# Kernel optimization log

Measured on AMD Instinct MI355X. Metric: run time of the kernel, lower is better.

The kernel has to match this reference:

```python
import jax, jax.numpy as jnp
import numpy as np

NEG_SLOPE = 0.2  # PyG GATConv default leaky_relu slope
EPS = 1e-16


def layer_norm(x, g, b):
    mu = x.mean(-1, keepdims=True)
    var = ((x - mu) ** 2).mean(-1, keepdims=True)
    return (x - mu) * jax.lax.rsqrt(var + 1e-5) * g + b


def gat_conv(x, src, dst, n, W, a_src, a_dst, bias):
    # x: [N, C_in]; W: [C_in, H*C]; a_src/a_dst: [H, C]; concat=False -> mean over heads
    H, C = a_src.shape
    xh = (x @ W).reshape(n, H, C)                      # [N, H, C]
    s_src = jnp.einsum('nhc,hc->nh', xh, a_src)         # [N, H]
    s_dst = jnp.einsum('nhc,hc->nh', xh, a_dst)         # [N, H]
    e = jax.nn.leaky_relu(s_src[src] + s_dst[dst], NEG_SLOPE)  # [E, H]
    # segment softmax over incoming edges of each destination node
    m = jax.ops.segment_max(e, dst, num_segments=n)     # [N, H]
    ee = jnp.exp(e - m[dst])
    z = jax.ops.segment_sum(ee, dst, num_segments=n)    # [N, H]
    alpha = ee / (z[dst] + EPS)                         # [E, H]
    msg = xh[src] * alpha[:, :, None]                   # [E, H, C]
    out = jax.ops.segment_sum(msg, dst, num_segments=n) # [N, H, C]
    return out.mean(axis=1) + bias                      # [N, C]


def setup_inputs() -> dict:
    key = jax.random.key(0)
    N, E, C, H, L = 50000, 400000, 64, 4, 2
    ks = jax.random.split(key, 16)
    x = jax.random.normal(ks[0], (N, C), dtype=jnp.float32)
    edge_index = jax.random.randint(ks[1], (2, E), 0, N, dtype=jnp.int64)
    sc = 1.0 / np.sqrt(C)
    return {
        'x': x,
        'edge_index': edge_index,
        'Wg': jax.random.normal(ks[2], (L, C, H * C), dtype=jnp.float32) * sc,
        'att_src': jax.random.normal(ks[3], (L, H, C), dtype=jnp.float32) * sc,
        'att_dst': jax.random.normal(ks[4], (L, H, C), dtype=jnp.float32) * sc,
        'att_bias': jnp.zeros((L, C), dtype=jnp.float32),
        'ln1_g': jnp.ones((L, C), dtype=jnp.float32),
        'ln1_b': jnp.zeros((L, C), dtype=jnp.float32),
        'W1': jax.random.normal(ks[5], (L, C, C), dtype=jnp.float32) * sc,
        'b1': jnp.zeros((L, C), dtype=jnp.float32),
        'W2': jax.random.normal(ks[6], (L, C, C), dtype=jnp.float32) * sc,
        'b2': jnp.zeros((L, C), dtype=jnp.float32),
        'ln2_g': jnp.ones((L, C), dtype=jnp.float32),
        'ln2_b': jnp.zeros((L, C), dtype=jnp.float32),
    }


def reference(x, edge_index, Wg, att_src, att_dst, att_bias,
              ln1_g, ln1_b, W1, b1, W2, b2, ln2_g, ln2_b):
    n = x.shape[0]
    L = Wg.shape[0]
    # PyG GATConv adds self loops by default
    loops = jnp.arange(n, dtype=edge_index.dtype)
    src = jnp.concatenate([edge_index[0], loops])
    dst = jnp.concatenate([edge_index[1], loops])
    for i in range(L):
        x_att = gat_conv(x, src, dst, n, Wg[i], att_src[i], att_dst[i], att_bias[i])
        x = layer_norm(x + x_att, ln1_g[i], ln1_b[i])
        h = jax.nn.relu(x @ W1[i] + b1[i])
        h = h @ W2[i] + b2[i]
        x = layer_norm(x + h, ln2_g[i], ln2_b[i])
    return x
```

## Files before the change

### kernel.cpp

```cpp
#include <hip/hip_runtime.h>
#include <hip/hip_bf16.h>
#include <float.h>

#define C 64
#define H 4
#define HC 256
#define NEG_SLOPE 0.2f
#define EPS_SEG 1e-16f
#define LN_EPS 1e-5f
#define LDSP 528

typedef __attribute__((ext_vector_type(8))) short bf16x8;
typedef __attribute__((ext_vector_type(4))) float f32x4;

__device__ __forceinline__ float warp_sum(float v) {
#pragma unroll
    for (int m = 32; m >= 1; m >>= 1) v += __shfl_xor(v, m, 64);
    return v;
}

__device__ __forceinline__ unsigned short f2bf(float f) {
    unsigned int u = __float_as_uint(f);
    return (unsigned short)((u + 0x7FFF + ((u >> 16) & 1)) >> 16);
}


__global__ void k_zero(int* __restrict__ a, int n) {
    int i = blockIdx.x * blockDim.x + threadIdx.x;
    int stride = gridDim.x * blockDim.x;
    for (int j = i; j < n; j += stride) a[j] = 0;
}

__global__ void k_count(const int* __restrict__ ei, int* __restrict__ counts,
                        int E, int Etot) {
    int eid = blockIdx.x * blockDim.x + threadIdx.x;
    if (eid >= Etot) return;
    int d = (eid < E) ? ei[E + eid] : eid - E;
    atomicAdd(&counts[d], 1);
}

__global__ __launch_bounds__(256) void k_scan1(const int* __restrict__ counts,
                                               int* __restrict__ tmp,
                                               int* __restrict__ bsum, int N) {
    __shared__ int sm[256];
    int t = threadIdx.x;
    int i = blockIdx.x * 256 + t;
    sm[t] = (i < N) ? counts[i] : 0;
    __syncthreads();
    for (int off = 1; off < 256; off <<= 1) {
        int add = (t >= off) ? sm[t - off] : 0;
        __syncthreads();
        sm[t] += add;
        __syncthreads();
    }
    if (i < N) tmp[i] = sm[t];
    if (t == 255) bsum[blockIdx.x] = sm[255];
}

__global__ __launch_bounds__(256) void k_scan2(int* __restrict__ bsum, int nb) {
    __shared__ int sm[256];
    int t = threadIdx.x;
    sm[t] = (t < nb) ? bsum[t] : 0;
    __syncthreads();
    for (int off = 1; off < 256; off <<= 1) {
        int add = (t >= off) ? sm[t - off] : 0;
        __syncthreads();
        sm[t] += add;
        __syncthreads();
    }
    if (t < nb) bsum[t] = (t > 0) ? sm[t - 1] : 0;
}

__global__ __launch_bounds__(256) void k_scan3(const int* __restrict__ tmp,
                                               const int* __restrict__ boff,
                                               int* __restrict__ rowptr,
                                               int* __restrict__ cursor, int N) {
    int i = blockIdx.x * 256 + threadIdx.x;
    if (i < N) {
        rowptr[i + 1] = tmp[i] + boff[blockIdx.x];
        cursor[i] = 0;
    }
    if (i == 0) rowptr[0] = 0;
}

__global__ void k_fill(const int* __restrict__ ei, const int* __restrict__ rowptr,
                       int* __restrict__ cursor, int* __restrict__ col,
                       int E, int Etot) {
    int eid = blockIdx.x * blockDim.x + threadIdx.x;
    if (eid >= Etot) return;
    int s, d;
    if (eid < E) { s = ei[eid]; d = ei[E + eid]; } else { s = d = eid - E; }
    int pos = rowptr[d] + atomicAdd(&cursor[d], 1);
    col[pos] = s;
}


__global__ void k_prep_x(const float4* __restrict__ xin, ushort4* __restrict__ xb,
                         int n4, int npad4) {
    int i = blockIdx.x * blockDim.x + threadIdx.x;
    int st = gridDim.x * blockDim.x;
    for (int j = i; j < npad4; j += st) {
        ushort4 o;
        if (j < n4) {
            float4 v = xin[j];
            o.x = f2bf(v.x); o.y = f2bf(v.y); o.z = f2bf(v.z); o.w = f2bf(v.w);
        } else {
            o.x = o.y = o.z = o.w = 0;
        }
        xb[j] = o;
    }
}

__global__ void k_prep_weights(const float* __restrict__ Wg,
                               const float* __restrict__ W1, const float* __restrict__ W2,
                               unsigned short* __restrict__ Wgt,
                               unsigned short* __restrict__ W1t,
                               unsigned short* __restrict__ W2t, int L) {
    int i = blockIdx.x * 256 + threadIdx.x;
    int nWg = L * C * HC;
    int nW = L * C * C;
    if (i < nWg) {
        int l = i / (C * HC);
        int r = i - l * C * HC;
        int n = r >> 6, k = r & 63;
        Wgt[(size_t)l * HC * C + n * C + k] = f2bf(Wg[(size_t)l * C * HC + k * HC + n]);
    } else if (i < nWg + nW) {
        int j = i - nWg;
        int l = j / (C * C);
        int r = j - l * C * C;
        int n = r >> 6, k = r & 63;
        W1t[(size_t)l * C * C + n * C + k] = f2bf(W1[(size_t)l * C * C + k * C + n]);
        W2t[(size_t)l * C * C + n * C + k] = f2bf(W2[(size_t)l * C * C + k * C + n]);
    }
}

__global__ __launch_bounds__(256) void k_gemm_mfma(
    const unsigned short* __restrict__ xb, const unsigned short* __restrict__ Wgt,
    const float* __restrict__ a_src, const float* __restrict__ a_dst,
    unsigned short* __restrict__ xh, float* __restrict__ s_src,
    float* __restrict__ s_dst, int N)
{
    __shared__ char tile[64 * LDSP];
    int w = threadIdx.x >> 6, l = threadIdx.x & 63;
    int n0 = blockIdx.x * 64;
    int lr = l & 15, q = l >> 4, lk = q * 8;
    bf16x8 bfr[4][2];
    float as[4], ad[4];
#pragma unroll
    for (int ct = 0; ct < 4; ct++) {
        int colg = w * 64 + ct * 16 + lr;
#pragma unroll
        for (int ks = 0; ks < 2; ks++)
            bfr[ct][ks] = *reinterpret_cast<const bf16x8*>(Wgt + colg * C + ks * 32 + lk);
        as[ct] = a_src[w * C + ct * 16 + lr];
        ad[ct] = a_dst[w * C + ct * 16 + lr];
    }
#pragma unroll
    for (int rt = 0; rt < 4; rt++) {
        const unsigned short* arow = xb + (size_t)(n0 + rt * 16 + lr) * C + lk;
        bf16x8 a0 = *reinterpret_cast<const bf16x8*>(arow);
        bf16x8 a1 = *reinterpret_cast<const bf16x8*>(arow + 32);
        f32x4 acc[4];
#pragma unroll
        for (int ct = 0; ct < 4; ct++) {
            acc[ct] = (f32x4){0.f, 0.f, 0.f, 0.f};
            acc[ct] = __builtin_amdgcn_mfma_f32_16x16x32_bf16(a0, bfr[ct][0], acc[ct], 0, 0, 0);
            acc[ct] = __builtin_amdgcn_mfma_f32_16x16x32_bf16(a1, bfr[ct][1], acc[ct], 0, 0, 0);
        }
        int rowl = rt * 16 + q * 4;
#pragma unroll
        for (int ct = 0; ct < 4; ct++) {
            int cb = (w * 64 + ct * 16 + lr) * 2;
#pragma unroll
            for (int r = 0; r < 4; r++)
                *(unsigned short*)(tile + (rowl + r) * LDSP + cb) = f2bf(acc[ct][r]);
        }
#pragma unroll
        for (int r = 0; r < 4; r++) {
            float ps = acc[0][r] * as[0] + acc[1][r] * as[1]
                     + acc[2][r] * as[2] + acc[3][r] * as[3];
            float pd = acc[0][r] * ad[0] + acc[1][r] * ad[1]
                     + acc[2][r] * ad[2] + acc[3][r] * ad[3];
#pragma unroll
            for (int off = 1; off < 16; off <<= 1) {
                ps += __shfl_xor(ps, off, 64);
                pd += __shfl_xor(pd, off, 64);
            }
            if (lr == 0) {
                int n = n0 + rowl + r;
                s_src[(size_t)n * H + w] = ps;
                s_dst[(size_t)n * H + w] = pd;
            }
        }
    }
    __syncthreads();
#pragma unroll
    for (int it = 0; it < 8; it++) {
        int off = threadIdx.x * 16 + it * 4096;
        int row = off >> 9;
        int cin = off & 511;
        uint4 v = *(const uint4*)(tile + row * LDSP + cin);
        *(uint4*)((char*)xh + (size_t)(n0 + row) * 512 + cin) = v;
    }
}

__global__ __launch_bounds__(256) void k_gat_node(
    const int* __restrict__ rowptr, const int* __restrict__ col,
    const float* __restrict__ s_src, const float* __restrict__ s_dst,
    const unsigned short* __restrict__ xh,
    const float* __restrict__ x_in, const float* __restrict__ bias,
    const float* __restrict__ g, const float* __restrict__ b,
    float* __restrict__ x1, unsigned short* __restrict__ x1b, int N)
{
    int n = (blockIdx.x * blockDim.x + threadIdx.x) >> 6;
    int l = threadIdx.x & 63;
    int h = l >> 4, gq = l & 15;
    if (n >= N) return;
    int r0 = rowptr[n], r1 = rowptr[n + 1];

    float4 xi = *(const float4*)(x_in + (size_t)n * C + gq * 4);
    float4 bia = *(const float4*)(bias + gq * 4);
    float sdh = s_dst[n * H + h];

    const char* xbase = (const char*)xh;
    int laneoff = h * 128 + gq * 8;

    float a0 = 0.f, a1 = 0.f, a2 = 0.f, a3 = 0.f, z = 0.f;

    int j = r0;
    for (; j + 4 <= r1; j += 4) {
        int s0 = col[j], s1 = col[j + 1], s2 = col[j + 2], s3 = col[j + 3];
        uint2 v0 = *(const uint2*)(xbase + (size_t)s0 * 512 + laneoff);
        uint2 v1 = *(const uint2*)(xbase + (size_t)s1 * 512 + laneoff);
        uint2 v2 = *(const uint2*)(xbase + (size_t)s2 * 512 + laneoff);
        uint2 v3 = *(const uint2*)(xbase + (size_t)s3 * 512 + laneoff);
        float e0 = s_src[s0 * H + h] + sdh;
        float e1 = s_src[s1 * H + h] + sdh;
        float e2 = s_src[s2 * H + h] + sdh;
        float e3 = s_src[s3 * H + h] + sdh;
        float w0 = __expf(fmaxf(e0, NEG_SLOPE * e0));
        float w1 = __expf(fmaxf(e1, NEG_SLOPE * e1));
        float w2 = __expf(fmaxf(e2, NEG_SLOPE * e2));
        float w3 = __expf(fmaxf(e3, NEG_SLOPE * e3));
        a0 += w0 * __uint_as_float(v0.x << 16);
        a1 += w0 * __uint_as_float(v0.x & 0xFFFF0000u);
        a2 += w0 * __uint_as_float(v0.y << 16);
        a3 += w0 * __uint_as_float(v0.y & 0xFFFF0000u);
        a0 += w1 * __uint_as_float(v1.x << 16);
        a1 += w1 * __uint_as_float(v1.x & 0xFFFF0000u);
        a2 += w1 * __uint_as_float(v1.y << 16);
        a3 += w1 * __uint_as_float(v1.y & 0xFFFF0000u);
        a0 += w2 * __uint_as_float(v2.x << 16);
        a1 += w2 * __uint_as_float(v2.x & 0xFFFF0000u);
        a2 += w2 * __uint_as_float(v2.y << 16);
        a3 += w2 * __uint_as_float(v2.y & 0xFFFF0000u);
        a0 += w3 * __uint_as_float(v3.x << 16);
        a1 += w3 * __uint_as_float(v3.x & 0xFFFF0000u);
        a2 += w3 * __uint_as_float(v3.y << 16);
        a3 += w3 * __uint_as_float(v3.y & 0xFFFF0000u);
        z += w0 + w1 + w2 + w3;
    }
    {
        int t = r1 - j;
        int s0 = 0, s1 = 0, s2 = 0;
        if (t > 0) s0 = col[j];
        if (t > 1) s1 = col[j + 1];
        if (t > 2) s2 = col[j + 2];
        uint2 v0 = {0, 0}, v1 = {0, 0}, v2 = {0, 0};
        float e0 = 0.f, e1 = 0.f, e2 = 0.f;
        if (t > 0) { v0 = *(const uint2*)(xbase + (size_t)s0 * 512 + laneoff); e0 = s_src[s0 * H + h] + sdh; }
        if (t > 1) { v1 = *(const uint2*)(xbase + (size_t)s1 * 512 + laneoff); e1 = s_src[s1 * H + h] + sdh; }
        if (t > 2) { v2 = *(const uint2*)(xbase + (size_t)s2 * 512 + laneoff); e2 = s_src[s2 * H + h] + sdh; }
        float w0 = (t > 0) ? __expf(fmaxf(e0, NEG_SLOPE * e0)) : 0.f;
        float w1 = (t > 1) ? __expf(fmaxf(e1, NEG_SLOPE * e1)) : 0.f;
        float w2 = (t > 2) ? __expf(fmaxf(e2, NEG_SLOPE * e2)) : 0.f;
        a0 += w0 * __uint_as_float(v0.x << 16);
        a1 += w0 * __uint_as_float(v0.x & 0xFFFF0000u);
        a2 += w0 * __uint_as_float(v0.y << 16);
        a3 += w0 * __uint_as_float(v0.y & 0xFFFF0000u);
        a0 += w1 * __uint_as_float(v1.x << 16);
        a1 += w1 * __uint_as_float(v1.x & 0xFFFF0000u);
        a2 += w1 * __uint_as_float(v1.y << 16);
        a3 += w1 * __uint_as_float(v1.y & 0xFFFF0000u);
        a0 += w2 * __uint_as_float(v2.x << 16);
        a1 += w2 * __uint_as_float(v2.x & 0xFFFF0000u);
        a2 += w2 * __uint_as_float(v2.y << 16);
        a3 += w2 * __uint_as_float(v2.y & 0xFFFF0000u);
        z += w0 + w1 + w2;
    }

    float inv = 0.25f / (z + EPS_SEG);
    a0 *= inv; a1 *= inv; a2 *= inv; a3 *= inv;
#pragma unroll
    for (int off = 16; off <= 32; off <<= 1) {
        a0 += __shfl_xor(a0, off, 64);
        a1 += __shfl_xor(a1, off, 64);
        a2 += __shfl_xor(a2, off, 64);
        a3 += __shfl_xor(a3, off, 64);
    }
    float y0 = xi.x + a0 + bia.x;
    float y1 = xi.y + a1 + bia.y;
    float y2 = xi.z + a2 + bia.z;
    float y3 = xi.w + a3 + bia.w;
    float mu = warp_sum(y0 + y1 + y2 + y3) * (1.f / (C * 4));
    float d0 = y0 - mu, d1 = y1 - mu, d2 = y2 - mu, d3 = y3 - mu;
    float var = warp_sum(d0 * d0 + d1 * d1 + d2 * d2 + d3 * d3) * (1.f / (C * 4));
    float rs = rsqrtf(var + LN_EPS);
    if (h == 0) {
        float4 gg = *(const float4*)(g + gq * 4);
        float4 bb = *(const float4*)(b + gq * 4);
        float4 o;
        o.x = d0 * rs * gg.x + bb.x;
        o.y = d1 * rs * gg.y + bb.y;
        o.z = d2 * rs * gg.z + bb.z;
        o.w = d3 * rs * gg.w + bb.w;
        *(float4*)(x1 + (size_t)n * C + gq * 4) = o;
        ushort4 ob;
        ob.x = f2bf(o.x); ob.y = f2bf(o.y); ob.z = f2bf(o.z); ob.w = f2bf(o.w);
        *(ushort4*)(x1b + (size_t)n * C + gq * 4) = ob;
    }
}

__global__ __launch_bounds__(256) void k_ffn_mfma(
    const float* __restrict__ x1f, const unsigned short* __restrict__ x1b,
    const unsigned short* __restrict__ W1t, const unsigned short* __restrict__ W2t,
    const float* __restrict__ b1, const float* __restrict__ b2,
    const float* __restrict__ g, const float* __restrict__ b,
    float* __restrict__ xout, unsigned short* __restrict__ xb, int N)
{
    __shared__ unsigned short hls[64 * 64];
    int w = threadIdx.x >> 6, l = threadIdx.x & 63;
    int lr = l & 15, q = l >> 4, lk = q * 8;
    int n0 = blockIdx.x * 64;

    {
        bf16x8 bf[4][2];
#pragma unroll
        for (int ct = 0; ct < 4; ct++)
#pragma unroll
            for (int ks = 0; ks < 2; ks++)
                bf[ct][ks] = *reinterpret_cast<const bf16x8*>(
                    W1t + (ct * 16 + lr) * C + ks * 32 + lk);
        const unsigned short* arow = x1b + (size_t)(n0 + w * 16 + lr) * C + lk;
        bf16x8 a0 = *reinterpret_cast<const bf16x8*>(arow);
        bf16x8 a1 = *reinterpret_cast<const bf16x8*>(arow + 32);
        f32x4 acc[4];
#pragma unroll
        for (int ct = 0; ct < 4; ct++) {
            acc[ct] = (f32x4){0.f, 0.f, 0.f, 0.f};
            acc[ct] = __builtin_amdgcn_mfma_f32_16x16x32_bf16(a0, bf[ct][0], acc[ct], 0, 0, 0);
            acc[ct] = __builtin_amdgcn_mfma_f32_16x16x32_bf16(a1, bf[ct][1], acc[ct], 0, 0, 0);
        }
#pragma unroll
        for (int ct = 0; ct < 4; ct++) {
            float bc = b1[ct * 16 + lr];
#pragma unroll
            for (int r = 0; r < 4; r++) {
                float v = fmaxf(acc[ct][r] + bc, 0.f);
                int rowb = w * 16 + q * 4 + r;
                int byte = rowb * 128 + (ct * 16 + lr) * 2;
                byte ^= (rowb & 7) << 4;
                *(unsigned short*)((char*)hls + byte) = f2bf(v);
            }
        }
    }
    __syncthreads();

    bf16x8 bf[4][2];
#pragma unroll
    for (int ct = 0; ct < 4; ct++)
#pragma unroll
        for (int ks = 0; ks < 2; ks++)
            bf[ct][ks] = *reinterpret_cast<const bf16x8*>(
                W2t + (ct * 16 + lr) * C + ks * 32 + lk);
    bf16x8 h0, h1;
    {
        int rowb = w * 16 + lr;
        int swz = (rowb & 7) << 4;
        int byte0 = (rowb * 128 + q * 16) ^ swz;
        int byte1 = (rowb * 128 + 64 + q * 16) ^ swz;
        h0 = *(bf16x8*)((char*)hls + byte0);
        h1 = *(bf16x8*)((char*)hls + byte1);
    }
    f32x4 acc[4];
#pragma unroll
    for (int ct = 0; ct < 4; ct++) {
        acc[ct] = (f32x4){0.f, 0.f, 0.f, 0.f};
        acc[ct] = __builtin_amdgcn_mfma_f32_16x16x32_bf16(h0, bf[ct][0], acc[ct], 0, 0, 0);
        acc[ct] = __builtin_amdgcn_mfma_f32_16x16x32_bf16(h1, bf[ct][1], acc[ct], 0, 0, 0);
    }

    float b2c[4], gc[4], bc[4];
#pragma unroll
    for (int ct = 0; ct < 4; ct++) {
        int cg = ct * 16 + lr;
        b2c[ct] = b2[cg]; gc[ct] = g[cg]; bc[ct] = b[cg];
    }
    float yv[4][4];
#pragma unroll
    for (int r = 0; r < 4; r++) {
        int n = n0 + w * 16 + q * 4 + r;
        bool ok = n < N;
#pragma unroll
        for (int ct = 0; ct < 4; ct++) {
            float xr = ok ? x1f[(size_t)n * C + ct * 16 + lr] : 0.f;
            yv[ct][r] = acc[ct][r] + b2c[ct] + xr;
        }
    }
#pragma unroll
    for (int r = 0; r < 4; r++) {
        int n = n0 + w * 16 + q * 4 + r;
        float s = yv[0][r] + yv[1][r] + yv[2][r] + yv[3][r];
#pragma unroll
        for (int off = 1; off < 16; off <<= 1) s += __shfl_xor(s, off, 64);
        float mu = s * (1.f / C);
        float d0 = yv[0][r] - mu, d1 = yv[1][r] - mu;
        float d2 = yv[2][r] - mu, d3 = yv[3][r] - mu;
        float vs = d0 * d0 + d1 * d1 + d2 * d2 + d3 * d3;
#pragma unroll
        for (int off = 1; off < 16; off <<= 1) vs += __shfl_xor(vs, off, 64);
        float rs = rsqrtf(vs * (1.f / C) + LN_EPS);
        if (n < N) {
            float dd[4] = {d0, d1, d2, d3};
#pragma unroll
            for (int ct = 0; ct < 4; ct++) {
                float o = dd[ct] * rs * gc[ct] + bc[ct];
                xout[(size_t)n * C + ct * 16 + lr] = o;
                xb[(size_t)n * C + ct * 16 + lr] = f2bf(o);
            }
        }
    }
}

extern "C" void kernel_launch(void* const* d_in, const int* in_sizes, int n_in,
                              void* d_out, int out_size, void* d_ws, size_t ws_size,
                              hipStream_t stream) {
    const float* x        = (const float*)d_in[0];
    const int*   ei       = (const int*)d_in[1];
    const float* Wg       = (const float*)d_in[2];
    const float* a_src    = (const float*)d_in[3];
    const float* a_dst    = (const float*)d_in[4];
    const float* att_bias = (const float*)d_in[5];
    const float* ln1_g    = (const float*)d_in[6];
    const float* ln1_b    = (const float*)d_in[7];
    const float* W1       = (const float*)d_in[8];
    const float* b1       = (const float*)d_in[9];
    const float* W2       = (const float*)d_in[10];
    const float* b2       = (const float*)d_in[11];
    const float* ln2_g    = (const float*)d_in[12];
    const float* ln2_b    = (const float*)d_in[13];
    float* xout = (float*)d_out;

    int N = in_sizes[0] / C;
    int E = in_sizes[1] / 2;
    int Etot = E + N;
    int L = in_sizes[2] / (C * HC);
    int nb = (N + 255) / 256;
    int Npad = (N + 63) & ~63;

    char* p = (char*)d_ws;
    auto alloc = [&](size_t bytes) { void* r = (void*)p; p += (bytes + 255) & ~(size_t)255; return r; };
    float* s_src = (float*)alloc((size_t)Npad * H * 4);
    float* s_dst = (float*)alloc((size_t)Npad * H * 4);
    float* x1    = (float*)alloc((size_t)N * C * 4);
    int* rowptr  = (int*)alloc((size_t)(N + 1) * 4);
    int* col     = (int*)alloc((size_t)Etot * 4);
    int* counts  = (int*)alloc((size_t)N * 4);
    int* tmp     = (int*)alloc((size_t)N * 4);
    int* bsum    = (int*)alloc((size_t)nb * 4);
    unsigned short* xb  = (unsigned short*)alloc((size_t)Npad * C * 2);
    unsigned short* x1b = (unsigned short*)alloc((size_t)Npad * C * 2);
    unsigned short* Wgt = (unsigned short*)alloc((size_t)L * HC * C * 2);
    unsigned short* W1t = (unsigned short*)alloc((size_t)L * C * C * 2);
    unsigned short* W2t = (unsigned short*)alloc((size_t)L * C * C * 2);
    unsigned short* xh  = (unsigned short*)alloc((size_t)Npad * HC * 2);

    k_zero<<<256, 256, 0, stream>>>(counts, N);
    k_count<<<(Etot + 255) / 256, 256, 0, stream>>>(ei, counts, E, Etot);
    k_scan1<<<nb, 256, 0, stream>>>(counts, tmp, bsum, N);
    k_scan2<<<1, 256, 0, stream>>>(bsum, nb);
    k_scan3<<<nb, 256, 0, stream>>>(tmp, bsum, rowptr, counts, N);
    k_fill<<<(Etot + 255) / 256, 256, 0, stream>>>(ei, rowptr, counts, col, E, Etot);
    k_prep_x<<<2048, 256, 0, stream>>>((const float4*)x, (ushort4*)xb,
                                       N * C / 4, Npad * C / 4);
    {
        int tot = L * C * HC + L * C * C;
        k_prep_weights<<<(tot + 255) / 256, 256, 0, stream>>>(Wg, W1, W2, Wgt, W1t, W2t, L);
    }

    for (int l = 0; l < L; l++) {
        const float* xin = (l == 0) ? x : xout;
        k_gemm_mfma<<<Npad / 64, 256, 0, stream>>>(
            xb, Wgt + (size_t)l * HC * C, a_src + l * H * C, a_dst + l * H * C,
            xh, s_src, s_dst, N);
        k_gat_node<<<(N + 3) / 4, 256, 0, stream>>>(
            rowptr, col, s_src, s_dst, xh, xin,
            att_bias + l * C, ln1_g + l * C, ln1_b + l * C, x1, x1b, N);
        k_ffn_mfma<<<Npad / 64, 256, 0, stream>>>(
            x1, x1b, W1t + (size_t)l * C * C, W2t + (size_t)l * C * C,
            b1 + l * C, b2 + l * C, ln2_g + l * C, ln2_b + l * C, xout, xb, N);
    }
}
```

Baseline: 212.3 us.

## Process GAT destination nodes in descending-degree order via counting-sort permutation

Adds a degree histogram, a serial bin scan, and an atomic scatter that build a permutation of nodes sorted by in-degree, high to low. The GAT aggregation kernel then maps each wavefront to perm[wid] instead of to node wid, so nodes of similar degree share a block and the heaviest nodes start first. This is meant to cut load imbalance and tail effects from the variable neighbor counts. The cost is three extra small kernel launches, and the x_in, x1 and xh row accesses become scattered rather than sequential, which can hurt memory locality.

```diff
diff --git a/kernel.cpp b/kernel.cpp
--- a/kernel.cpp
+++ b/kernel.cpp
@@ -37,6 +37,28 @@
     if (eid >= Etot) return;
     int d = (eid < E) ? ei[E + eid] : eid - E;
     atomicAdd(&counts[d], 1);
+}
+
+__global__ void k_hist(const int* __restrict__ counts, int* __restrict__ hist, int N) {
+    int i = blockIdx.x * blockDim.x + threadIdx.x;
+    if (i < N) atomicAdd(&hist[min(counts[i], 63)], 1);
+}
+
+__global__ void k_binscan(const int* __restrict__ hist, int* __restrict__ cursor) {
+    if (threadIdx.x == 0 && blockIdx.x == 0) {
+        int s = 0;
+        for (int d = 63; d >= 0; d--) { cursor[d] = s; s += hist[d]; }
+    }
+}
+
+__global__ void k_scatter(const int* __restrict__ counts, int* __restrict__ cursor,
+                          int* __restrict__ perm, int N) {
+    int i = blockIdx.x * blockDim.x + threadIdx.x;
+    if (i < N) {
+        int bin = min(counts[i], 63);
+        int pos = atomicAdd(&cursor[bin], 1);
+        perm[pos] = i;
+    }
 }
 
 __global__ __launch_bounds__(256) void k_scan1(const int* __restrict__ counts,
@@ -205,6 +227,7 @@
 }
 
 __global__ __launch_bounds__(256) void k_gat_node(
+    const int* __restrict__ perm,
     const int* __restrict__ rowptr, const int* __restrict__ col,
     const float* __restrict__ s_src, const float* __restrict__ s_dst,
     const unsigned short* __restrict__ xh,
@@ -212,10 +235,11 @@
     const float* __restrict__ g, const float* __restrict__ b,
     float* __restrict__ x1, unsigned short* __restrict__ x1b, int N)
 {
-    int n = (blockIdx.x * blockDim.x + threadIdx.x) >> 6;
+    int wid = (blockIdx.x * blockDim.x + threadIdx.x) >> 6;
     int l = threadIdx.x & 63;
     int h = l >> 4, gq = l & 15;
-    if (n >= N) return;
+    if (wid >= N) return;
+    int n = perm[wid];
     int r0 = rowptr[n], r1 = rowptr[n + 1];
 
     float4 xi = *(const float4*)(x_in + (size_t)n * C + gq * 4);
@@ -465,7 +489,10 @@
     float* x1    = (float*)alloc((size_t)N * C * 4);
     int* rowptr  = (int*)alloc((size_t)(N + 1) * 4);
     int* col     = (int*)alloc((size_t)Etot * 4);
-    int* counts  = (int*)alloc((size_t)N * 4);
+    int* counts  = (int*)alloc((size_t)(N + 128) * 4);
+    int* hist    = counts + N;
+    int* cursor  = counts + N + 64;
+    int* perm    = (int*)alloc((size_t)N * 4);
     int* tmp     = (int*)alloc((size_t)N * 4);
     int* bsum    = (int*)alloc((size_t)nb * 4);
     unsigned short* xb  = (unsigned short*)alloc((size_t)Npad * C * 2);
@@ -475,8 +502,11 @@
     unsigned short* W2t = (unsigned short*)alloc((size_t)L * C * C * 2);
     unsigned short* xh  = (unsigned short*)alloc((size_t)Npad * HC * 2);
 
-    k_zero<<<256, 256, 0, stream>>>(counts, N);
+    k_zero<<<256, 256, 0, stream>>>(counts, N + 128);
     k_count<<<(Etot + 255) / 256, 256, 0, stream>>>(ei, counts, E, Etot);
+    k_hist<<<(N + 255) / 256, 256, 0, stream>>>(counts, hist, N);
+    k_binscan<<<1, 64, 0, stream>>>(hist, cursor);
+    k_scatter<<<(N + 255) / 256, 256, 0, stream>>>(counts, cursor, perm, N);
     k_scan1<<<nb, 256, 0, stream>>>(counts, tmp, bsum, N);
     k_scan2<<<1, 256, 0, stream>>>(bsum, nb);
     k_scan3<<<nb, 256, 0, stream>>>(tmp, bsum, rowptr, counts, N);
@@ -494,7 +524,7 @@
             xb, Wgt + (size_t)l * HC * C, a_src + l * H * C, a_dst + l * H * C,
             xh, s_src, s_dst, N);
         k_gat_node<<<(N + 3) / 4, 256, 0, stream>>>(
-            rowptr, col, s_src, s_dst, xh, xin,
+            perm, rowptr, col, s_src, s_dst, xh, xin,
             att_bias + l * C, ln1_g + l * C, ln1_b + l * C, x1, x1b, N);
         k_ffn_mfma<<<Npad / 64, 256, 0, stream>>>(
             x1, x1b, W1t + (size_t)l * C * C, W2t + (size_t)l * C * C,
```

Result: slower. 561.1 us (+164.3%).

## Fuse FFN of layer l with next layer's GAT projection GEMM

Applied to the files above, without the earlier changes.

Adds a kernel that runs the FFN plus second layer norm and then, keeping the normalized bf16 tile in shared memory, immediately computes the next layer's x@Wg projection and attention scores. This drops one kernel launch per layer boundary and avoids writing and re-reading the bf16 copy of x between kernels. The final layer still uses the plain FFN kernel, which no longer writes the bf16 output. The cost is higher shared memory use per block, which may lower occupancy.

```diff
diff --git a/kernel.cpp b/kernel.cpp
--- a/kernel.cpp
+++ b/kernel.cpp
@@ -326,7 +326,7 @@
     const unsigned short* __restrict__ W1t, const unsigned short* __restrict__ W2t,
     const float* __restrict__ b1, const float* __restrict__ b2,
     const float* __restrict__ g, const float* __restrict__ b,
-    float* __restrict__ xout, unsigned short* __restrict__ xb, int N)
+    float* __restrict__ xout, int N)
 {
     __shared__ unsigned short hls[64 * 64];
     int w = threadIdx.x >> 6, l = threadIdx.x & 63;
@@ -358,8 +358,7 @@
             for (int r = 0; r < 4; r++) {
                 float v = fmaxf(acc[ct][r] + bc, 0.f);
                 int rowb = w * 16 + q * 4 + r;
-                int byte = rowb * 128 + (ct * 16 + lr) * 2;
-                byte ^= (rowb & 7) << 4;
+                int byte = (rowb * 128 + (ct * 16 + lr) * 2) ^ ((rowb & 7) << 4);
                 *(unsigned short*)((char*)hls + byte) = f2bf(v);
             }
         }
@@ -377,10 +376,8 @@
     {
         int rowb = w * 16 + lr;
         int swz = (rowb & 7) << 4;
-        int byte0 = (rowb * 128 + q * 16) ^ swz;
-        int byte1 = (rowb * 128 + 64 + q * 16) ^ swz;
-        h0 = *(bf16x8*)((char*)hls + byte0);
-        h1 = *(bf16x8*)((char*)hls + byte1);
+        h0 = *(bf16x8*)((char*)hls + ((rowb * 128 + q * 16) ^ swz));
+        h1 = *(bf16x8*)((char*)hls + ((rowb * 128 + 64 + q * 16) ^ swz));
     }
     f32x4 acc[4];
 #pragma unroll
@@ -426,9 +423,186 @@
             for (int ct = 0; ct < 4; ct++) {
                 float o = dd[ct] * rs * gc[ct] + bc[ct];
                 xout[(size_t)n * C + ct * 16 + lr] = o;
-                xb[(size_t)n * C + ct * 16 + lr] = f2bf(o);
-            }
-        }
+            }
+        }
+    }
+}
+
+__global__ __launch_bounds__(256) void k_ffn_gemm(
+    const float* __restrict__ x1f, const unsigned short* __restrict__ x1b,
+    const unsigned short* __restrict__ W1t, const unsigned short* __restrict__ W2t,
+    const float* __restrict__ b1, const float* __restrict__ b2,
+    const float* __restrict__ g, const float* __restrict__ b,
+    const unsigned short* __restrict__ Wgt2,
+    const float* __restrict__ a_src2, const float* __restrict__ a_dst2,
+    float* __restrict__ xout, unsigned short* __restrict__ xh,
+    float* __restrict__ s_src, float* __restrict__ s_dst, int N)
+{
+    __shared__ char tile[64 * LDSP];
+    __shared__ unsigned short hls[64 * 64];
+    int w = threadIdx.x >> 6, l = threadIdx.x & 63;
+    int lr = l & 15, q = l >> 4, lk = q * 8;
+    int n0 = blockIdx.x * 64;
+
+    {
+        bf16x8 bf[4][2];
+#pragma unroll
+        for (int ct = 0; ct < 4; ct++)
+#pragma unroll
+            for (int ks = 0; ks < 2; ks++)
+                bf[ct][ks] = *reinterpret_cast<const bf16x8*>(
+                    W1t + (ct * 16 + lr) * C + ks * 32 + lk);
+        const unsigned short* arow = x1b + (size_t)(n0 + w * 16 + lr) * C + lk;
+        bf16x8 a0 = *reinterpret_cast<const bf16x8*>(arow);
+        bf16x8 a1 = *reinterpret_cast<const bf16x8*>(arow + 32);
+        f32x4 acc[4];
+#pragma unroll
+        for (int ct = 0; ct < 4; ct++) {
+            acc[ct] = (f32x4){0.f, 0.f, 0.f, 0.f};
+            acc[ct] = __builtin_amdgcn_mfma_f32_16x16x32_bf16(a0, bf[ct][0], acc[ct], 0, 0, 0);
+            acc[ct] = __builtin_amdgcn_mfma_f32_16x16x32_bf16(a1, bf[ct][1], acc[ct], 0, 0, 0);
+        }
+#pragma unroll
+        for (int ct = 0; ct < 4; ct++) {
+            float bc = b1[ct * 16 + lr];
+#pragma unroll
+            for (int r = 0; r < 4; r++) {
+                float v = fmaxf(acc[ct][r] + bc, 0.f);
+                int rowb = w * 16 + q * 4 + r;
+                int byte = (rowb * 128 + (ct * 16 + lr) * 2) ^ ((rowb & 7) << 4);
+                *(unsigned short*)((char*)hls + byte) = f2bf(v);
+            }
+        }
+    }
+    __syncthreads();
+
+    {
+        bf16x8 bf[4][2];
+#pragma unroll
+        for (int ct = 0; ct < 4; ct++)
+#pragma unroll
+            for (int ks = 0; ks < 2; ks++)
+                bf[ct][ks] = *reinterpret_cast<const bf16x8*>(
+                    W2t + (ct * 16 + lr) * C + ks * 32 + lk);
+        bf16x8 h0, h1;
+        {
+            int rowb = w * 16 + lr;
+            int swz = (rowb & 7) << 4;
+            h0 = *(bf16x8*)((char*)hls + ((rowb * 128 + q * 16) ^ swz));
+            h1 = *(bf16x8*)((char*)hls + ((rowb * 128 + 64 + q * 16) ^ swz));
+        }
+        __syncthreads();
+        f32x4 acc[4];
+#pragma unroll
+        for (int ct = 0; ct < 4; ct++) {
+            acc[ct] = (f32x4){0.f, 0.f, 0.f, 0.f};
+            acc[ct] = __builtin_amdgcn_mfma_f32_16x16x32_bf16(h0, bf[ct][0], acc[ct], 0, 0, 0);
+            acc[ct] = __builtin_amdgcn_mfma_f32_16x16x32_bf16(h1, bf[ct][1], acc[ct], 0, 0, 0);
+        }
+        float b2c[4], gc[4], bc[4];
+#pragma unroll
+        for (int ct = 0; ct < 4; ct++) {
+            int cg = ct * 16 + lr;
+            b2c[ct] = b2[cg]; gc[ct] = g[cg]; bc[ct] = b[cg];
+        }
+        float yv[4][4];
+#pragma unroll
+        for (int r = 0; r < 4; r++) {
+            int n = n0 + w * 16 + q * 4 + r;
+            bool ok = n < N;
+#pragma unroll
+            for (int ct = 0; ct < 4; ct++) {
+                float xr = ok ? x1f[(size_t)n * C + ct * 16 + lr] : 0.f;
+                yv[ct][r] = acc[ct][r] + b2c[ct] + xr;
+            }
+        }
+#pragma unroll
+        for (int r = 0; r < 4; r++) {
+            int rowb = w * 16 + q * 4 + r;
+            int n = n0 + rowb;
+            bool ok = n < N;
+            float s = yv[0][r] + yv[1][r] + yv[2][r] + yv[3][r];
+#pragma unroll
+            for (int off = 1; off < 16; off <<= 1) s += __shfl_xor(s, off, 64);
+            float mu = s * (1.f / C);
+            float d0 = yv[0][r] - mu, d1 = yv[1][r] - mu;
+            float d2 = yv[2][r] - mu, d3 = yv[3][r] - mu;
+            float vs = d0 * d0 + d1 * d1 + d2 * d2 + d3 * d3;
+#pragma unroll
+            for (int off = 1; off < 16; off <<= 1) vs += __shfl_xor(vs, off, 64);
+            float rs = rsqrtf(vs * (1.f / C) + LN_EPS);
+            float dd[4] = {d0, d1, d2, d3};
+#pragma unroll
+            for (int ct = 0; ct < 4; ct++) {
+                float o = dd[ct] * rs * gc[ct] + bc[ct];
+                if (ok) xout[(size_t)n * C + ct * 16 + lr] = o;
+                int byte = (rowb * 128 + (ct * 16 + lr) * 2) ^ ((rowb & 7) << 4);
+                *(unsigned short*)((char*)hls + byte) = ok ? f2bf(o) : 0;
+            }
+        }
+    }
+    __syncthreads();
+
+    {
+        bf16x8 bfr[4][2];
+        float as[4], ad[4];
+#pragma unroll
+        for (int ct = 0; ct < 4; ct++) {
+            int colg = w * 64 + ct * 16 + lr;
+#pragma unroll
+            for (int ks = 0; ks < 2; ks++)
+                bfr[ct][ks] = *reinterpret_cast<const bf16x8*>(Wgt2 + colg * C + ks * 32 + lk);
+            as[ct] = a_src2[w * C + ct * 16 + lr];
+            ad[ct] = a_dst2[w * C + ct * 16 + lr];
+        }
+#pragma unroll
+        for (int rt = 0; rt < 4; rt++) {
+            int arowb = rt * 16 + lr;
+            int aswz = (arowb & 7) << 4;
+            bf16x8 ga0 = *(bf16x8*)((char*)hls + ((arowb * 128 + q * 16) ^ aswz));
+            bf16x8 ga1 = *(bf16x8*)((char*)hls + ((arowb * 128 + 64 + q * 16) ^ aswz));
+            f32x4 acc[4];
+#pragma unroll
+            for (int ct = 0; ct < 4; ct++) {
+                acc[ct] = (f32x4){0.f, 0.f, 0.f, 0.f};
+                acc[ct] = __builtin_amdgcn_mfma_f32_16x16x32_bf16(ga0, bfr[ct][0], acc[ct], 0, 0, 0);
+                acc[ct] = __builtin_amdgcn_mfma_f32_16x16x32_bf16(ga1, bfr[ct][1], acc[ct], 0, 0, 0);
+            }
+            int rowl = rt * 16 + q * 4;
+#pragma unroll
+            for (int ct = 0; ct < 4; ct++) {
+                int cb = (w * 64 + ct * 16 + lr) * 2;
+#pragma unroll
+                for (int r = 0; r < 4; r++)
+                    *(unsigned short*)(tile + (rowl + r) * LDSP + cb) = f2bf(acc[ct][r]);
+            }
+#pragma unroll
+            for (int r = 0; r < 4; r++) {
+                float ps = acc[0][r] * as[0] + acc[1][r] * as[1]
+                         + acc[2][r] * as[2] + acc[3][r] * as[3];
+                float pd = acc[0][r] * ad[0] + acc[1][r] * ad[1]
+                         + acc[2][r] * ad[2] + acc[3][r] * ad[3];
+#pragma unroll
+                for (int off = 1; off < 16; off <<= 1) {
+                    ps += __shfl_xor(ps, off, 64);
+                    pd += __shfl_xor(pd, off, 64);
+                }
+                if (lr == 0) {
+                    int n = n0 + rowl + r;
+                    s_src[(size_t)n * H + w] = ps;
+                    s_dst[(size_t)n * H + w] = pd;
+                }
+            }
+        }
+    }
+    __syncthreads();
+#pragma unroll
+    for (int it = 0; it < 8; it++) {
+        int off = threadIdx.x * 16 + it * 4096;
+        int row = off >> 9;
+        int cin = off & 511;
+        uint4 v = *(const uint4*)(tile + row * LDSP + cin);
+        *(uint4*)((char*)xh + (size_t)(n0 + row) * 512 + cin) = v;
     }
 }
 
@@ -490,14 +664,22 @@
 
     for (int l = 0; l < L; l++) {
         const float* xin = (l == 0) ? x : xout;
-        k_gemm_mfma<<<Npad / 64, 256, 0, stream>>>(
-            xb, Wgt + (size_t)l * HC * C, a_src + l * H * C, a_dst + l * H * C,
-            xh, s_src, s_dst, N);
+        if (l == 0)
+            k_gemm_mfma<<<Npad / 64, 256, 0, stream>>>(
+                xb, Wgt, a_src, a_dst, xh, s_src, s_dst, N);
         k_gat_node<<<(N + 3) / 4, 256, 0, stream>>>(
             rowptr, col, s_src, s_dst, xh, xin,
             att_bias + l * C, ln1_g + l * C, ln1_b + l * C, x1, x1b, N);
-        k_ffn_mfma<<<Npad / 64, 256, 0, stream>>>(
-            x1, x1b, W1t + (size_t)l * C * C, W2t + (size_t)l * C * C,
-            b1 + l * C, b2 + l * C, ln2_g + l * C, ln2_b + l * C, xout, xb, N);
-    }
-}
+        if (l < L - 1)
+            k_ffn_gemm<<<Npad / 64, 256, 0, stream>>>(
+                x1, x1b, W1t + (size_t)l * C * C, W2t + (size_t)l * C * C,
+                b1 + l * C, b2 + l * C, ln2_g + l * C, ln2_b + l * C,
+                Wgt + (size_t)(l + 1) * HC * C,
+                a_src + (size_t)(l + 1) * H * C, a_dst + (size_t)(l + 1) * H * C,
+                xout, xh, s_src, s_dst, N);
+        else
+            k_ffn_mfma<<<Npad / 64, 256, 0, stream>>>(
+                x1, x1b, W1t + (size_t)l * C * C, W2t + (size_t)l * C * C,
+                b1 + l * C, b2 + l * C, ln2_g + l * C, ln2_b + l * C, xout, N);
+    }
+}
```

Result: no change. 210.0 us, median of 2 (-1.0%).
